# Optimization experiments

Hardware: AMD Instinct MI355X
Metric: run time of the kernel (lower is better)

## Reference

```python
import jax, jax.numpy as jnp
import numpy as np

N = 256  # node_num, fully-connected graph
NEG_SLOPE = 0.2


def _edges(n):
    # fully-connected permutations; PyG GATConv removes then re-adds self-loops,
    # so effectively all n*n (src, dst) pairs are present.
    idx = jnp.arange(n)
    src = jnp.repeat(idx, n)
    dst = jnp.tile(idx, n)
    return src, dst


def _gat_conv(x, W, att_src, att_dst, b, src, dst, n):
    # x: [N, Fin], W: [Fin, H*C], att_*: [H, C], b: [H*C]
    H, C = att_src.shape
    h = (x @ W).reshape(n, H, C)                       # [N, H, C]
    a_src = jnp.einsum('nhc,hc->nh', h, att_src)       # [N, H]
    a_dst = jnp.einsum('nhc,hc->nh', h, att_dst)
    e = jax.nn.leaky_relu(a_src[src] + a_dst[dst], NEG_SLOPE)  # [E, H]
    # segment softmax over incoming edges of each dst node
    m = jax.ops.segment_max(e, dst, num_segments=n)    # [N, H]
    p = jnp.exp(e - m[dst])
    denom = jax.ops.segment_sum(p, dst, num_segments=n)
    alpha = p / (denom[dst] + 1e-16)                   # [E, H]
    msg = h[src] * alpha[:, :, None]                   # [E, H, C]
    out = jax.ops.segment_sum(msg, dst, num_segments=n)  # [N, H, C]
    return out.reshape(n, H * C) + b


def setup_inputs() -> dict:
    key = jax.random.key(0)
    ks = jax.random.split(key, 7)
    Fin, H1, C1 = 128, 4, 128
    s = lambda fan: 1.0 / np.sqrt(fan)
    return {
        'x': jax.random.normal(ks[0], (8, N, Fin), dtype=jnp.float32),
        'W1': jax.random.normal(ks[1], (Fin, H1 * C1), dtype=jnp.float32) * s(Fin),
        'att_src1': jax.random.normal(ks[2], (H1, C1), dtype=jnp.float32) * s(C1),
        'att_dst1': jax.random.normal(ks[3], (H1, C1), dtype=jnp.float32) * s(C1),
        'b1': jnp.zeros((H1 * C1,), dtype=jnp.float32),
        'W2': jax.random.normal(ks[4], (H1 * C1, Fin), dtype=jnp.float32) * s(H1 * C1),
        'att_src2': jax.random.normal(ks[5], (1, Fin), dtype=jnp.float32) * s(Fin),
        'att_dst2': jax.random.normal(ks[6], (1, Fin), dtype=jnp.float32) * s(Fin),
        'b2': jnp.zeros((Fin,), dtype=jnp.float32),
    }


def reference(x, W1, att_src1, att_dst1, b1, W2, att_src2, att_dst2, b2):
    src, dst = _edges(N)

    def one_graph(xi):
        h = jax.nn.relu(_gat_conv(xi, W1, att_src1, att_dst1, b1, src, dst, N))
        return _gat_conv(h, W2, att_src2, att_dst2, b2, src, dst, N)

    return jax.vmap(one_graph)(x)  # [B, N, Fin]
```

## Files before the change

### kernel.cpp

```cpp
#include <hip/hip_runtime.h>
#include <hip/hip_bf16.h>

#define BATCH 8
#define NN    256
#define FIN   128
#define H1    4
#define C1    128
#define HC1   512
#define NEG_SLOPE 0.2f

__device__ __forceinline__ float lrelu(float v) {
    return v > 0.f ? v : NEG_SLOPE * v;
}

__global__ __launch_bounds__(512, 4)
void gemm1_fused(const float* __restrict__ x, const float* __restrict__ W1,
                 const float* __restrict__ as1, const float* __restrict__ ad1,
                 float* __restrict__ h1, float* __restrict__ a_src,
                 float* __restrict__ a_dst) {
    __shared__ float xs[4][FIN];
    __shared__ float redS[4][8], redD[4][8];
    const int b = blockIdx.y, r0 = blockIdx.x * 4, t = threadIdx.x;

    if (t < 128)
        ((float4*)xs)[t] = ((const float4*)(x + (size_t)(b * NN + r0) * FIN))[t];
    __syncthreads();

    float a0 = 0.f, a1 = 0.f, a2 = 0.f, a3 = 0.f;
    #pragma unroll 8
    for (int k = 0; k < FIN; ++k) {
        float w = W1[k * HC1 + t];
        a0 = fmaf(xs[0][k], w, a0);
        a1 = fmaf(xs[1][k], w, a1);
        a2 = fmaf(xs[2][k], w, a2);
        a3 = fmaf(xs[3][k], w, a3);
    }
    float acc[4] = {a0, a1, a2, a3};
    #pragma unroll
    for (int r = 0; r < 4; ++r)
        h1[(b * NN + r0 + r) * HC1 + t] = acc[r];

    const float as = as1[t], ad = ad1[t];
    const int w = t >> 6, lane = t & 63;
    #pragma unroll
    for (int r = 0; r < 4; ++r) {
        float s = acc[r] * as, d = acc[r] * ad;
        #pragma unroll
        for (int off = 32; off > 0; off >>= 1) {
            s += __shfl_down(s, off, 64);
            d += __shfl_down(d, off, 64);
        }
        if (lane == 0) { redS[r][w] = s; redD[r][w] = d; }
    }
    __syncthreads();
    if (t < 16) {
        int r = t & 3, h = t >> 2;
        a_src[(b * NN + r0 + r) * H1 + h] = redS[r][2 * h] + redS[r][2 * h + 1];
        a_dst[(b * NN + r0 + r) * H1 + h] = redD[r][2 * h] + redD[r][2 * h + 1];
    }
}

__global__ __launch_bounds__(512, 2)
void mid_fused(const float* __restrict__ h1, const float* __restrict__ a_src,
               const float* __restrict__ a_dst, const float* __restrict__ b1,
               const float* __restrict__ W2, const float* __restrict__ as2,
               const float* __restrict__ ad2, float* __restrict__ h2,
               float* __restrict__ a_src2, float* __restrict__ a_dst2) {
    __shared__ __align__(16) float s_as[H1][NN];
    __shared__ float s_ad[H1][8];
    __shared__ __align__(16) float spT[NN][36];
    __shared__ float s_den[32];
    __shared__ __align__(16) float hrelu_s[8][HC1];
    __shared__ float red[3][8][FIN];
    __shared__ float redS[8][2], redD[8][2];

    const int b = blockIdx.y, d0 = blockIdx.x * 8, t = threadIdx.x;

    {
        int i0 = t, i1 = t + 512;
        ((float*)s_as)[ (i0 >> 8) * NN + (i0 & 255) ] = a_src[(b * NN + (i0 & 255)) * H1 + (i0 >> 8)];
        ((float*)s_as)[ (i1 >> 8) * NN + (i1 & 255) ] = a_src[(b * NN + (i1 & 255)) * H1 + (i1 >> 8)];
        if (t < 32) {
            int h = t >> 3, d = t & 7;
            s_ad[h][d] = a_dst[(b * NN + d0 + d) * H1 + h];
        }
    }
    __syncthreads();

    {
        const int pair = t >> 4, sub = t & 15;
        const int h = pair >> 3, d = pair & 7;
        const float adst = s_ad[h][d];
        float e[16];
        float mx = -1e30f;
        #pragma unroll
        for (int i = 0; i < 16; ++i) {
            float v = lrelu(s_as[h][sub + i * 16] + adst);
            e[i] = v;
            mx = fmaxf(mx, v);
        }
        #pragma unroll
        for (int off = 8; off > 0; off >>= 1)
            mx = fmaxf(mx, __shfl_down(mx, off, 16));
        mx = __shfl(mx, 0, 16);
        float sum = 0.f;
        #pragma unroll
        for (int i = 0; i < 16; ++i) {
            float p = __expf(e[i] - mx);
            spT[sub + i * 16][pair] = p;
            sum += p;
        }
        #pragma unroll
        for (int off = 8; off > 0; off >>= 1)
            sum += __shfl_down(sum, off, 16);
        if (sub == 0) s_den[pair] = sum + 1e-16f;
    }
    __syncthreads();

    {
        const int ct = t, h = t >> 7;
        float acc8[8] = {0,0,0,0,0,0,0,0};
        const float* hb = h1 + (size_t)(b * NN) * HC1 + ct;
        #pragma unroll 4
        for (int src = 0; src < NN; ++src) {
            float hv = hb[(size_t)src * HC1];
            float4 pa = *(const float4*)&spT[src][h * 8];
            float4 pb = *(const float4*)&spT[src][h * 8 + 4];
            acc8[0] = fmaf(pa.x, hv, acc8[0]);
            acc8[1] = fmaf(pa.y, hv, acc8[1]);
            acc8[2] = fmaf(pa.z, hv, acc8[2]);
            acc8[3] = fmaf(pa.w, hv, acc8[3]);
            acc8[4] = fmaf(pb.x, hv, acc8[4]);
            acc8[5] = fmaf(pb.y, hv, acc8[5]);
            acc8[6] = fmaf(pb.z, hv, acc8[6]);
            acc8[7] = fmaf(pb.w, hv, acc8[7]);
        }
        const float bias = b1[ct];
        #pragma unroll
        for (int d = 0; d < 8; ++d)
            hrelu_s[d][ct] = fmaxf(acc8[d] / s_den[h * 8 + d] + bias, 0.f);
    }
    __syncthreads();

    const int c2 = t & 127, g = t >> 7;
    float acc[8] = {0,0,0,0,0,0,0,0};
    {
        const float* wb = W2 + (size_t)(g * 128) * FIN + c2;
        #pragma unroll 2
        for (int kq = 0; kq < 32; ++kq) {
            float w0 = wb[(size_t)(kq * 4 + 0) * FIN];
            float w1 = wb[(size_t)(kq * 4 + 1) * FIN];
            float w2 = wb[(size_t)(kq * 4 + 2) * FIN];
            float w3 = wb[(size_t)(kq * 4 + 3) * FIN];
            #pragma unroll
            for (int r = 0; r < 8; ++r) {
                float4 xv = *(const float4*)&hrelu_s[r][g * 128 + kq * 4];
                acc[r] = fmaf(xv.x, w0, acc[r]);
                acc[r] = fmaf(xv.y, w1, acc[r]);
                acc[r] = fmaf(xv.z, w2, acc[r]);
                acc[r] = fmaf(xv.w, w3, acc[r]);
            }
        }
    }
    if (g > 0) {
        #pragma unroll
        for (int r = 0; r < 8; ++r) red[g - 1][r][c2] = acc[r];
    }
    __syncthreads();
    if (g == 0) {
        #pragma unroll
        for (int r = 0; r < 8; ++r) {
            acc[r] += red[0][r][c2] + red[1][r][c2] + red[2][r][c2];
            h2[(b * NN + d0 + r) * FIN + c2] = acc[r];
        }
        const int lane = t & 63, wv = t >> 6;
        const float as = as2[c2], ad = ad2[c2];
        #pragma unroll
        for (int r = 0; r < 8; ++r) {
            float s = acc[r] * as, dd = acc[r] * ad;
            #pragma unroll
            for (int off = 32; off > 0; off >>= 1) {
                s += __shfl_down(s, off, 64);
                dd += __shfl_down(dd, off, 64);
            }
            if (lane == 0) { redS[r][wv] = s; redD[r][wv] = dd; }
        }
    }
    __syncthreads();
    if (t < 8) {
        a_src2[b * NN + d0 + t] = redS[t][0] + redS[t][1];
        a_dst2[b * NN + d0 + t] = redD[t][0] + redD[t][1];
    }
}

__global__ __launch_bounds__(512, 4)
void agg2_kernel(const float* __restrict__ h2, const float* __restrict__ a_src,
                 const float* __restrict__ a_dst, const float* __restrict__ b2,
                 float* __restrict__ out) {
    __shared__ float s_as[NN];
    __shared__ float s_ad[4];
    __shared__ float sp[4][NN];
    __shared__ float redm[4][2], reds[4][2];
    __shared__ float s_den[4];
    __shared__ float redA[3][4][FIN];

    const int b = blockIdx.y, d0 = blockIdx.x * 4, t = threadIdx.x;

    if (t < NN) s_as[t] = a_src[b * NN + t];
    if (t < 4) s_ad[t] = a_dst[b * NN + d0 + t];
    __syncthreads();

    const int d = t >> 7, l = t & 127, lane = t & 63, w = (t >> 6) & 1;
    const float adst = s_ad[d];
    float e0 = lrelu(s_as[l] + adst);
    float e1 = lrelu(s_as[l + 128] + adst);
    float mx = fmaxf(e0, e1);
    #pragma unroll
    for (int off = 32; off > 0; off >>= 1)
        mx = fmaxf(mx, __shfl_down(mx, off, 64));
    if (lane == 0) redm[d][w] = mx;
    __syncthreads();
    const float m = fmaxf(redm[d][0], redm[d][1]);
    float p0 = __expf(e0 - m), p1 = __expf(e1 - m);
    sp[d][l] = p0;
    sp[d][l + 128] = p1;
    float sum = p0 + p1;
    #pragma unroll
    for (int off = 32; off > 0; off >>= 1)
        sum += __shfl_down(sum, off, 64);
    if (lane == 0) reds[d][w] = sum;
    __syncthreads();
    if (t < 4) s_den[t] = reds[t][0] + reds[t][1] + 1e-16f;
    __syncthreads();

    const int c = l, q = d;
    float a4[4] = {0.f, 0.f, 0.f, 0.f};
    const float* hb = h2 + ((size_t)(b * NN) + q * 64) * FIN + c;
    #pragma unroll 8
    for (int i = 0; i < 64; ++i) {
        float hv = hb[(size_t)i * FIN];
        int src = q * 64 + i;
        a4[0] = fmaf(sp[0][src], hv, a4[0]);
        a4[1] = fmaf(sp[1][src], hv, a4[1]);
        a4[2] = fmaf(sp[2][src], hv, a4[2]);
        a4[3] = fmaf(sp[3][src], hv, a4[3]);
    }
    if (q > 0) {
        #pragma unroll
        for (int j = 0; j < 4; ++j) redA[q - 1][j][c] = a4[j];
    }
    __syncthreads();
    if (q == 0) {
        #pragma unroll
        for (int j = 0; j < 4; ++j) {
            float v = a4[j] + redA[0][j][c] + redA[1][j][c] + redA[2][j][c];
            out[(b * NN + d0 + j) * FIN + c] = v / s_den[j] + b2[c];
        }
    }
}

extern "C" void kernel_launch(void* const* d_in, const int* in_sizes, int n_in,
                              void* d_out, int out_size, void* d_ws, size_t ws_size,
                              hipStream_t stream) {
    const float* x   = (const float*)d_in[0];
    const float* W1  = (const float*)d_in[1];
    const float* as1 = (const float*)d_in[2];
    const float* ad1 = (const float*)d_in[3];
    const float* b1  = (const float*)d_in[4];
    const float* W2  = (const float*)d_in[5];
    const float* as2 = (const float*)d_in[6];
    const float* ad2 = (const float*)d_in[7];
    const float* b2  = (const float*)d_in[8];
    float* out = (float*)d_out;

    float* ws = (float*)d_ws;
    float* h1     = ws;
    float* h2     = ws + 1048576;
    float* a_src1 = ws + 1310720;
    float* a_dst1 = ws + 1318912;
    float* a_src2 = ws + 1327104;
    float* a_dst2 = ws + 1329152;

    gemm1_fused<<<dim3(64, BATCH), 512, 0, stream>>>(x, W1, as1, ad1, h1, a_src1, a_dst1);
    mid_fused<<<dim3(32, BATCH), 512, 0, stream>>>(h1, a_src1, a_dst1, b1, W2, as2, ad2,
                                                   h2, a_src2, a_dst2);
    agg2_kernel<<<dim3(64, BATCH), 512, 0, stream>>>(h2, a_src2, a_dst2, b2, out);
}
```

Measured before the change: 117.7 us.

## Merge three GAT kernels into one cooperative kernel with grid syncs

Replaces the three separate kernel launches with a single cooperative kernel of 256 blocks that runs the three stages and separates them with grid.sync(). The stages reuse one shared memory pool, and the first GEMM and final aggregation now process 8 rows per block instead of 4. This is meant to remove launch overhead and the gaps between kernels. In exchange it adds the cost of grid-wide barriers and gives the first and last stages half as many blocks.

```diff
diff --git a/kernel.cpp b/kernel.cpp
--- a/kernel.cpp
+++ b/kernel.cpp
@@ -1,5 +1,7 @@
 #include <hip/hip_runtime.h>
-#include <hip/hip_bf16.h>
+#include <hip/hip_cooperative_groups.h>
+
+namespace cg = cooperative_groups;
 
 #define BATCH 8
 #define NN    256
@@ -13,119 +15,246 @@
     return v > 0.f ? v : NEG_SLOPE * v;
 }
 
-__global__ __launch_bounds__(512, 4)
-void gemm1_fused(const float* __restrict__ x, const float* __restrict__ W1,
-                 const float* __restrict__ as1, const float* __restrict__ ad1,
-                 float* __restrict__ h1, float* __restrict__ a_src,
-                 float* __restrict__ a_dst) {
-    __shared__ float xs[4][FIN];
-    __shared__ float redS[4][8], redD[4][8];
-    const int b = blockIdx.y, r0 = blockIdx.x * 4, t = threadIdx.x;
-
-    if (t < 128)
-        ((float4*)xs)[t] = ((const float4*)(x + (size_t)(b * NN + r0) * FIN))[t];
-    __syncthreads();
-
-    float a0 = 0.f, a1 = 0.f, a2 = 0.f, a3 = 0.f;
-    #pragma unroll 8
-    for (int k = 0; k < FIN; ++k) {
-        float w = W1[k * HC1 + t];
-        a0 = fmaf(xs[0][k], w, a0);
-        a1 = fmaf(xs[1][k], w, a1);
-        a2 = fmaf(xs[2][k], w, a2);
-        a3 = fmaf(xs[3][k], w, a3);
+#define POOL_FLOATS 17504
+
+__global__ __launch_bounds__(512, 2)
+void gat_all(const float* __restrict__ x,   const float* __restrict__ W1,
+             const float* __restrict__ as1, const float* __restrict__ ad1,
+             const float* __restrict__ b1,  const float* __restrict__ W2,
+             const float* __restrict__ as2, const float* __restrict__ ad2,
+             const float* __restrict__ b2,  float* __restrict__ out,
+             float* __restrict__ h1, float* __restrict__ h2,
+             float* __restrict__ aS1, float* __restrict__ aD1,
+             float* __restrict__ aS2, float* __restrict__ aD2) {
+    __shared__ __align__(16) float pool[POOL_FLOATS];
+    cg::grid_group grid = cg::this_grid();
+    const int blk = blockIdx.x, t = threadIdx.x;
+
+    {
+        float* xs = pool;
+        float* rS = pool + 1024;
+        float* rD = pool + 1088;
+        const int b = blk >> 5, rt = blk & 31;
+        const float* xp = x + ((size_t)b * NN + rt * 8) * FIN;
+        if (t < 256) ((float4*)xs)[t] = ((const float4*)xp)[t];
+        __syncthreads();
+
+        float acc[8] = {0,0,0,0,0,0,0,0};
+        #pragma unroll 4
+        for (int k = 0; k < FIN; ++k) {
+            float w = W1[(size_t)k * HC1 + t];
+            #pragma unroll
+            for (int r = 0; r < 8; ++r)
+                acc[r] = fmaf(xs[r * FIN + k], w, acc[r]);
+        }
+        #pragma unroll
+        for (int r = 0; r < 8; ++r)
+            h1[((size_t)b * NN + rt * 8 + r) * HC1 + t] = acc[r];
+
+        const float as = as1[t], ad = ad1[t];
+        const int w = t >> 6, lane = t & 63;
+        #pragma unroll
+        for (int r = 0; r < 8; ++r) {
+            float s = acc[r] * as, d = acc[r] * ad;
+            #pragma unroll
+            for (int off = 32; off > 0; off >>= 1) {
+                s += __shfl_down(s, off, 64);
+                d += __shfl_down(d, off, 64);
+            }
+            if (lane == 0) { rS[r * 8 + w] = s; rD[r * 8 + w] = d; }
+        }
+        __syncthreads();
+        if (t < 32) {
+            int r = t & 7, h = t >> 3;
+            size_t node = (size_t)b * NN + rt * 8 + r;
+            aS1[node * H1 + h] = rS[r * 8 + 2 * h] + rS[r * 8 + 2 * h + 1];
+            aD1[node * H1 + h] = rD[r * 8 + 2 * h] + rD[r * 8 + 2 * h + 1];
+        }
     }
-    float acc[4] = {a0, a1, a2, a3};
-    #pragma unroll
-    for (int r = 0; r < 4; ++r)
-        h1[(b * NN + r0 + r) * HC1 + t] = acc[r];
-
-    const float as = as1[t], ad = ad1[t];
-    const int w = t >> 6, lane = t & 63;
-    #pragma unroll
-    for (int r = 0; r < 4; ++r) {
-        float s = acc[r] * as, d = acc[r] * ad;
-        #pragma unroll
-        for (int off = 32; off > 0; off >>= 1) {
-            s += __shfl_down(s, off, 64);
-            d += __shfl_down(d, off, 64);
-        }
-        if (lane == 0) { redS[r][w] = s; redD[r][w] = d; }
+    grid.sync();
+
+    {
+        float* s_as  = pool;
+        float* s_ad  = pool + 1024;
+        float* spT   = pool + 1056;
+        float* s_den = pool + 10272;
+        float* hrelu = pool + 10304;
+        float* red   = pool + 14400;
+        float* redS  = pool + 17472;
+        float* redD  = pool + 17488;
+        const int b = blk >> 5, d0 = (blk & 31) * 8;
+
+        {
+            int i0 = t, i1 = t + 512;
+            s_as[(i0 >> 8) * NN + (i0 & 255)] =
+                aS1[((size_t)b * NN + (i0 & 255)) * H1 + (i0 >> 8)];
+            s_as[(i1 >> 8) * NN + (i1 & 255)] =
+                aS1[((size_t)b * NN + (i1 & 255)) * H1 + (i1 >> 8)];
+            if (t < 32) {
+                int h = t >> 3, d = t & 7;
+                s_ad[h * 8 + d] = aD1[((size_t)b * NN + d0 + d) * H1 + h];
+            }
+        }
+        __syncthreads();
+
+        {
+            const int pair = t >> 4, sub = t & 15;
+            const int h = pair >> 3, d = pair & 7;
+            const float adst = s_ad[h * 8 + d];
+            float e[16];
+            float mx = -1e30f;
+            #pragma unroll
+            for (int i = 0; i < 16; ++i) {
+                float v = lrelu(s_as[h * NN + sub + i * 16] + adst);
+                e[i] = v;
+                mx = fmaxf(mx, v);
+            }
+            #pragma unroll
+            for (int off = 8; off > 0; off >>= 1)
+                mx = fmaxf(mx, __shfl_down(mx, off, 16));
+            mx = __shfl(mx, 0, 16);
+            float sum = 0.f;
+            #pragma unroll
+            for (int i = 0; i < 16; ++i) {
+                float p = __expf(e[i] - mx);
+                spT[(sub + i * 16) * 36 + pair] = p;
+                sum += p;
+            }
+            #pragma unroll
+            for (int off = 8; off > 0; off >>= 1)
+                sum += __shfl_down(sum, off, 16);
+            if (sub == 0) s_den[pair] = sum + 1e-16f;
+        }
+        __syncthreads();
+
+        {
+            const int ct = t, h = t >> 7;
+            float acc8[8] = {0,0,0,0,0,0,0,0};
+            const float* hb = h1 + (size_t)(b * NN) * HC1 + ct;
+            #pragma unroll 4
+            for (int src = 0; src < NN; ++src) {
+                float hv = hb[(size_t)src * HC1];
+                float4 pa = *(const float4*)&spT[src * 36 + h * 8];
+                float4 pb = *(const float4*)&spT[src * 36 + h * 8 + 4];
+                acc8[0] = fmaf(pa.x, hv, acc8[0]);
+                acc8[1] = fmaf(pa.y, hv, acc8[1]);
+                acc8[2] = fmaf(pa.z, hv, acc8[2]);
+                acc8[3] = fmaf(pa.w, hv, acc8[3]);
+                acc8[4] = fmaf(pb.x, hv, acc8[4]);
+                acc8[5] = fmaf(pb.y, hv, acc8[5]);
+                acc8[6] = fmaf(pb.z, hv, acc8[6]);
+                acc8[7] = fmaf(pb.w, hv, acc8[7]);
+            }
+            const float bias = b1[ct];
+            #pragma unroll
+            for (int d = 0; d < 8; ++d)
+                hrelu[d * HC1 + ct] =
+                    fmaxf(acc8[d] / s_den[h * 8 + d] + bias, 0.f);
+        }
+        __syncthreads();
+
+        const int c2 = t & 127, g = t >> 7;
+        float acc[8] = {0,0,0,0,0,0,0,0};
+        {
+            const float* wb = W2 + (size_t)(g * 128) * FIN + c2;
+            #pragma unroll 2
+            for (int kq = 0; kq < 32; ++kq) {
+                float w0 = wb[(size_t)(kq * 4 + 0) * FIN];
+                float w1 = wb[(size_t)(kq * 4 + 1) * FIN];
+                float w2 = wb[(size_t)(kq * 4 + 2) * FIN];
+                float w3 = wb[(size_t)(kq * 4 + 3) * FIN];
+                #pragma unroll
+                for (int r = 0; r < 8; ++r) {
+                    float4 xv = *(const float4*)&hrelu[r * HC1 + g * 128 + kq * 4];
+                    acc[r] = fmaf(xv.x, w0, acc[r]);
+                    acc[r] = fmaf(xv.y, w1, acc[r]);
+                    acc[r] = fmaf(xv.z, w2, acc[r]);
+                    acc[r] = fmaf(xv.w, w3, acc[r]);
+                }
+            }
+        }
+        if (g > 0) {
+            #pragma unroll
+            for (int r = 0; r < 8; ++r) red[(g - 1) * 1024 + r * 128 + c2] = acc[r];
+        }
+        __syncthreads();
+        if (g == 0) {
+            #pragma unroll
+            for (int r = 0; r < 8; ++r) {
+                acc[r] += red[r * 128 + c2] + red[1024 + r * 128 + c2]
+                        + red[2048 + r * 128 + c2];
+                h2[((size_t)b * NN + d0 + r) * FIN + c2] = acc[r];
+            }
+            const int lane = t & 63, wv = t >> 6;
+            const float asv = as2[c2], adv = ad2[c2];
+            #pragma unroll
+            for (int r = 0; r < 8; ++r) {
+                float s = acc[r] * asv, dd = acc[r] * adv;
+                #pragma unroll
+                for (int off = 32; off > 0; off >>= 1) {
+                    s += __shfl_down(s, off, 64);
+                    dd += __shfl_down(dd, off, 64);
+                }
+                if (lane == 0) { redS[r * 2 + wv] = s; redD[r * 2 + wv] = dd; }
+            }
+        }
+        __syncthreads();
+        if (t < 8) {
+            aS2[(size_t)b * NN + d0 + t] = redS[t * 2] + redS[t * 2 + 1];
+            aD2[(size_t)b * NN + d0 + t] = redD[t * 2] + redD[t * 2 + 1];
+        }
     }
-    __syncthreads();
-    if (t < 16) {
-        int r = t & 3, h = t >> 2;
-        a_src[(b * NN + r0 + r) * H1 + h] = redS[r][2 * h] + redS[r][2 * h + 1];
-        a_dst[(b * NN + r0 + r) * H1 + h] = redD[r][2 * h] + redD[r][2 * h + 1];
-    }
-}
-
-__global__ __launch_bounds__(512, 2)
-void mid_fused(const float* __restrict__ h1, const float* __restrict__ a_src,
-               const float* __restrict__ a_dst, const float* __restrict__ b1,
-               const float* __restrict__ W2, const float* __restrict__ as2,
-               const float* __restrict__ ad2, float* __restrict__ h2,
-               float* __restrict__ a_src2, float* __restrict__ a_dst2) {
-    __shared__ __align__(16) float s_as[H1][NN];
-    __shared__ float s_ad[H1][8];
-    __shared__ __align__(16) float spT[NN][36];
-    __shared__ float s_den[32];
-    __shared__ __align__(16) float hrelu_s[8][HC1];
-    __shared__ float red[3][8][FIN];
-    __shared__ float redS[8][2], redD[8][2];
-
-    const int b = blockIdx.y, d0 = blockIdx.x * 8, t = threadIdx.x;
+    grid.sync();
 
     {
-        int i0 = t, i1 = t + 512;
-        ((float*)s_as)[ (i0 >> 8) * NN + (i0 & 255) ] = a_src[(b * NN + (i0 & 255)) * H1 + (i0 >> 8)];
-        ((float*)s_as)[ (i1 >> 8) * NN + (i1 & 255) ] = a_src[(b * NN + (i1 & 255)) * H1 + (i1 >> 8)];
-        if (t < 32) {
-            int h = t >> 3, d = t & 7;
-            s_ad[h][d] = a_dst[(b * NN + d0 + d) * H1 + h];
-        }
-    }
-    __syncthreads();
-
-    {
-        const int pair = t >> 4, sub = t & 15;
-        const int h = pair >> 3, d = pair & 7;
-        const float adst = s_ad[h][d];
-        float e[16];
-        float mx = -1e30f;
-        #pragma unroll
-        for (int i = 0; i < 16; ++i) {
-            float v = lrelu(s_as[h][sub + i * 16] + adst);
-            e[i] = v;
-            mx = fmaxf(mx, v);
-        }
-        #pragma unroll
-        for (int off = 8; off > 0; off >>= 1)
-            mx = fmaxf(mx, __shfl_down(mx, off, 16));
-        mx = __shfl(mx, 0, 16);
-        float sum = 0.f;
-        #pragma unroll
-        for (int i = 0; i < 16; ++i) {
-            float p = __expf(e[i] - mx);
-            spT[sub + i * 16][pair] = p;
-            sum += p;
-        }
-        #pragma unroll
-        for (int off = 8; off > 0; off >>= 1)
-            sum += __shfl_down(sum, off, 16);
-        if (sub == 0) s_den[pair] = sum + 1e-16f;
-    }
-    __syncthreads();
-
-    {
-        const int ct = t, h = t >> 7;
+        float* s_as3 = pool;
+        float* s_ad3 = pool + 256;
+        float* spT3  = pool + 272;
+        float* den3  = pool + 2320;
+        float* redA  = pool + 2336;
+        const int b = blk >> 5, d0 = (blk & 31) * 8;
+
+        if (t < NN) s_as3[t] = aS2[(size_t)b * NN + t];
+        if (t < 8)  s_ad3[t] = aD2[(size_t)b * NN + d0 + t];
+        __syncthreads();
+
+        {
+            const int d = t >> 6, lane = t & 63;
+            const float adst = s_ad3[d];
+            float e[4];
+            float mx = -1e30f;
+            #pragma unroll
+            for (int i = 0; i < 4; ++i) {
+                float v = lrelu(s_as3[lane + i * 64] + adst);
+                e[i] = v;
+                mx = fmaxf(mx, v);
+            }
+            #pragma unroll
+            for (int off = 32; off > 0; off >>= 1)
+                mx = fmaxf(mx, __shfl_down(mx, off, 64));
+            mx = __shfl(mx, 0, 64);
+            float sum = 0.f;
+            #pragma unroll
+            for (int i = 0; i < 4; ++i) {
+                float p = __expf(e[i] - mx);
+                spT3[(lane + i * 64) * 8 + d] = p;
+                sum += p;
+            }
+            #pragma unroll
+            for (int off = 32; off > 0; off >>= 1)
+                sum += __shfl_down(sum, off, 64);
+            if (lane == 0) den3[d] = sum + 1e-16f;
+        }
+        __syncthreads();
+
+        const int c = t & 127, q = t >> 7;
         float acc8[8] = {0,0,0,0,0,0,0,0};
-        const float* hb = h1 + (size_t)(b * NN) * HC1 + ct;
+        const float* hb = h2 + ((size_t)b * NN + q * 64) * FIN + c;
         #pragma unroll 4
-        for (int src = 0; src < NN; ++src) {
-            float hv = hb[(size_t)src * HC1];
-            float4 pa = *(const float4*)&spT[src][h * 8];
-            float4 pb = *(const float4*)&spT[src][h * 8 + 4];
+        for (int i = 0; i < 64; ++i) {
+            float hv = hb[(size_t)i * FIN];
+            float4 pa = *(const float4*)&spT3[(q * 64 + i) * 8];
+            float4 pb = *(const float4*)&spT3[(q * 64 + i) * 8 + 4];
             acc8[0] = fmaf(pa.x, hv, acc8[0]);
             acc8[1] = fmaf(pa.y, hv, acc8[1]);
             acc8[2] = fmaf(pa.z, hv, acc8[2]);
@@ -135,126 +264,19 @@
             acc8[6] = fmaf(pb.z, hv, acc8[6]);
             acc8[7] = fmaf(pb.w, hv, acc8[7]);
         }
-        const float bias = b1[ct];
-        #pragma unroll
-        for (int d = 0; d < 8; ++d)
-            hrelu_s[d][ct] = fmaxf(acc8[d] / s_den[h * 8 + d] + bias, 0.f);
-    }
-    __syncthreads();
-
-    const int c2 = t & 127, g = t >> 7;
-    float acc[8] = {0,0,0,0,0,0,0,0};
-    {
-        const float* wb = W2 + (size_t)(g * 128) * FIN + c2;
-        #pragma unroll 2
-        for (int kq = 0; kq < 32; ++kq) {
-            float w0 = wb[(size_t)(kq * 4 + 0) * FIN];
-            float w1 = wb[(size_t)(kq * 4 + 1) * FIN];
-            float w2 = wb[(size_t)(kq * 4 + 2) * FIN];
-            float w3 = wb[(size_t)(kq * 4 + 3) * FIN];
-            #pragma unroll
-            for (int r = 0; r < 8; ++r) {
-                float4 xv = *(const float4*)&hrelu_s[r][g * 128 + kq * 4];
-                acc[r] = fmaf(xv.x, w0, acc[r]);
-                acc[r] = fmaf(xv.y, w1, acc[r]);
-                acc[r] = fmaf(xv.z, w2, acc[r]);
-                acc[r] = fmaf(xv.w, w3, acc[r]);
-            }
-        }
-    }
-    if (g > 0) {
-        #pragma unroll
-        for (int r = 0; r < 8; ++r) red[g - 1][r][c2] = acc[r];
-    }
-    __syncthreads();
-    if (g == 0) {
-        #pragma unroll
-        for (int r = 0; r < 8; ++r) {
-            acc[r] += red[0][r][c2] + red[1][r][c2] + red[2][r][c2];
-            h2[(b * NN + d0 + r) * FIN + c2] = acc[r];
-        }
-        const int lane = t & 63, wv = t >> 6;
-        const float as = as2[c2], ad = ad2[c2];
-        #pragma unroll
-        for (int r = 0; r < 8; ++r) {
-            float s = acc[r] * as, dd = acc[r] * ad;
-            #pragma unroll
-            for (int off = 32; off > 0; off >>= 1) {
-                s += __shfl_down(s, off, 64);
-                dd += __shfl_down(dd, off, 64);
-            }
-            if (lane == 0) { redS[r][wv] = s; redD[r][wv] = dd; }
-        }
-    }
-    __syncthreads();
-    if (t < 8) {
-        a_src2[b * NN + d0 + t] = redS[t][0] + redS[t][1];
-        a_dst2[b * NN + d0 + t] = redD[t][0] + redD[t][1];
-    }
-}
-
-__global__ __launch_bounds__(512, 4)
-void agg2_kernel(const float* __restrict__ h2, const float* __restrict__ a_src,
-                 const float* __restrict__ a_dst, const float* __restrict__ b2,
-                 float* __restrict__ out) {
-    __shared__ float s_as[NN];
-    __shared__ float s_ad[4];
-    __shared__ float sp[4][NN];
-    __shared__ float redm[4][2], reds[4][2];
-    __shared__ float s_den[4];
-    __shared__ float redA[3][4][FIN];
-
-    const int b = blockIdx.y, d0 = blockIdx.x * 4, t = threadIdx.x;
-
-    if (t < NN) s_as[t] = a_src[b * NN + t];
-    if (t < 4) s_ad[t] = a_dst[b * NN + d0 + t];
-    __syncthreads();
-
-    const int d = t >> 7, l = t & 127, lane = t & 63, w = (t >> 6) & 1;
-    const float adst = s_ad[d];
-    float e0 = lrelu(s_as[l] + adst);
-    float e1 = lrelu(s_as[l + 128] + adst);
-    float mx = fmaxf(e0, e1);
-    #pragma unroll
-    for (int off = 32; off > 0; off >>= 1)
-        mx = fmaxf(mx, __shfl_down(mx, off, 64));
-    if (lane == 0) redm[d][w] = mx;
-    __syncthreads();
-    const float m = fmaxf(redm[d][0], redm[d][1]);
-    float p0 = __expf(e0 - m), p1 = __expf(e1 - m);
-    sp[d][l] = p0;
-    sp[d][l + 128] = p1;
-    float sum = p0 + p1;
-    #pragma unroll
-    for (int off = 32; off > 0; off >>= 1)
-        sum += __shfl_down(sum, off, 64);
-    if (lane == 0) reds[d][w] = sum;
-    __syncthreads();
-    if (t < 4) s_den[t] = reds[t][0] + reds[t][1] + 1e-16f;
-    __syncthreads();
-
-    const int c = l, q = d;
-    float a4[4] = {0.f, 0.f, 0.f, 0.f};
-    const float* hb = h2 + ((size_t)(b * NN) + q * 64) * FIN + c;
-    #pragma unroll 8
-    for (int i = 0; i < 64; ++i) {
-        float hv = hb[(size_t)i * FIN];
-        int src = q * 64 + i;
-        a4[0] = fmaf(sp[0][src], hv, a4[0]);
-        a4[1] = fmaf(sp[1][src], hv, a4[1]);
-        a4[2] = fmaf(sp[2][src], hv, a4[2]);
-        a4[3] = fmaf(sp[3][src], hv, a4[3]);
-    }
-    if (q > 0) {
-        #pragma unroll
-        for (int j = 0; j < 4; ++j) redA[q - 1][j][c] = a4[j];
-    }
-    __syncthreads();
-    if (q == 0) {
-        #pragma unroll
-        for (int j = 0; j < 4; ++j) {
-            float v = a4[j] + redA[0][j][c] + redA[1][j][c] + redA[2][j][c];
-            out[(b * NN + d0 + j) * FIN + c] = v / s_den[j] + b2[c];
+        if (q > 0) {
+            #pragma unroll
+            for (int j = 0; j < 8; ++j) redA[(q - 1) * 1024 + j * 128 + c] = acc8[j];
+        }
+        __syncthreads();
+        if (q == 0) {
+            const float bias = b2[c];
+            #pragma unroll
+            for (int j = 0; j < 8; ++j) {
+                float v = acc8[j] + redA[j * 128 + c] + redA[1024 + j * 128 + c]
+                        + redA[2048 + j * 128 + c];
+                out[((size_t)b * NN + d0 + j) * FIN + c] = v / den3[j] + bias;
+            }
         }
     }
 }
@@ -274,15 +296,18 @@
     float* out = (float*)d_out;
 
     float* ws = (float*)d_ws;
-    float* h1     = ws;
-    float* h2     = ws + 1048576;
-    float* a_src1 = ws + 1310720;
-    float* a_dst1 = ws + 1318912;
-    float* a_src2 = ws + 1327104;
-    float* a_dst2 = ws + 1329152;
-
-    gemm1_fused<<<dim3(64, BATCH), 512, 0, stream>>>(x, W1, as1, ad1, h1, a_src1, a_dst1);
-    mid_fused<<<dim3(32, BATCH), 512, 0, stream>>>(h1, a_src1, a_dst1, b1, W2, as2, ad2,
-                                                   h2, a_src2, a_dst2);
-    agg2_kernel<<<dim3(64, BATCH), 512, 0, stream>>>(h2, a_src2, a_dst2, b2, out);
+    float* h1  = ws;
+    float* h2  = ws + 1048576;
+    float* aS1 = ws + 1310720;
+    float* aD1 = ws + 1318912;
+    float* aS2 = ws + 1327104;
+    float* aD2 = ws + 1329152;
+
+    void* args[] = {
+        (void*)&x, (void*)&W1, (void*)&as1, (void*)&ad1, (void*)&b1,
+        (void*)&W2, (void*)&as2, (void*)&ad2, (void*)&b2, (void*)&out,
+        (void*)&h1, (void*)&h2, (void*)&aS1, (void*)&aD1, (void*)&aS2, (void*)&aD2
+    };
+    hipLaunchCooperativeKernel((const void*)gat_all, dim3(256), dim3(512),
+                               args, 0, stream);
 }
```

Result: slower. 187.7 us (+59.5%).
